# Optimization experiments

Measured on AMD Instinct MI355X. Metric: run time of the kernel, lower is better.

The kernel has to match this reference:

```python
import jax, jax.numpy as jnp
import numpy as np

N = 50000   # nodes
D = 128     # input_dim
E = 1600000 # edges
K = 100     # out_nodes


def setup_inputs() -> dict:
    key = jax.random.key(0)
    ks = jax.random.split(key, 9)
    x = jax.random.normal(ks[0], (N, D), dtype=jnp.float32)
    edge_index = jax.random.randint(ks[1], (2, E), 0, N, dtype=jnp.int64)
    # PyG GCNConv params: Linear(in,out,bias=False) weight + separate bias
    s = 1.0 / np.sqrt(D)
    W1 = jax.random.uniform(ks[2], (D, D), jnp.float32, -s, s)
    b1 = jnp.zeros((D,), jnp.float32)
    W2 = jax.random.uniform(ks[3], (D, D), jnp.float32, -s, s)
    b2 = jnp.zeros((D,), jnp.float32)
    Wa = jax.random.uniform(ks[4], (D, K), jnp.float32, -s, s)
    ba = jax.random.uniform(ks[5], (K,), jnp.float32, -s, s)
    return {"x": x, "edge_index": edge_index, "W1": W1, "b1": b1,
            "W2": W2, "b2": b2, "Wa": Wa, "ba": ba}


def _gcn_conv(x, src, dst, norm, W, b, n_nodes):
    # PyG GCNConv: h = x @ W; aggregate D^-1/2 (A+I) D^-1/2 h; add bias
    h = x @ W                                  # [N, D]
    msg = h[src] * norm[:, None]               # [E+N, D] gather + scale
    agg = jax.ops.segment_sum(msg, dst, num_segments=n_nodes)  # scatter-add
    return agg + b


def reference(x, edge_index, W1, b1, W2, b2, Wa, ba):
    n = x.shape[0]
    loop = jnp.arange(n, dtype=edge_index.dtype)
    src = jnp.concatenate([edge_index[0], loop])   # add self-loops
    dst = jnp.concatenate([edge_index[1], loop])
    deg = jnp.zeros((n,), x.dtype).at[dst].add(1.0)
    dinv = jnp.where(deg > 0, jax.lax.rsqrt(deg), 0.0)
    norm = dinv[src] * dinv[dst]                   # [E+N]

    h = _gcn_conv(x, src, dst, norm, W1, b1, n)
    h = jax.nn.relu(h)
    h = _gcn_conv(h, src, dst, norm, W2, b2, n)
    s = jax.nn.softmax(h @ Wa + ba, axis=1)        # [N, K]
    return s
```

## Files before the change

kernel.cpp:

```cpp
#include <hip/hip_runtime.h>

#define D 128
#define KOUT 100
#define CHUNK 4096

typedef __attribute__((ext_vector_type(8))) short short8;
typedef __attribute__((ext_vector_type(4))) float floatx4;

__device__ inline float bf_lo(unsigned int u) { return __uint_as_float(u << 16); }
__device__ inline float bf_hi(unsigned int u) { return __uint_as_float(u & 0xFFFF0000u); }

__device__ inline unsigned int bf_round(float a) {
    unsigned int ua = __float_as_uint(a);
    return (ua + 0x7FFFu + ((ua >> 16) & 1u)) >> 16;
}
__device__ inline unsigned int pack_bf(float a, float b) {
    return bf_round(a) | (bf_round(b) << 16);
}


__launch_bounds__(256)
__global__ void bucket_pass1(const int* __restrict__ ei, int E, int nbuck, int cap,
                             int* __restrict__ bcur, unsigned int* __restrict__ bdata) {
    __shared__ int hist[256];
    __shared__ int sc[256];
    __shared__ int pfx[256];
    __shared__ int cur[256];
    __shared__ int gbase[256];
    __shared__ unsigned int lbuf[CHUNK];
    __shared__ unsigned char bkt[CHUNK];

    int tid = threadIdx.x;
    int base = blockIdx.x * CHUNK;
    int cnt = E - base; if (cnt > CHUNK) cnt = CHUNK;

    hist[tid] = 0;
    __syncthreads();

    int src[CHUNK / 256];
    int dst[CHUNK / 256];
#pragma unroll
    for (int q = 0; q < CHUNK / 256; q++) {
        int li = tid + q * 256;
        if (li < cnt) {
            src[q] = ei[base + li];
            dst[q] = ei[E + base + li];
            atomicAdd(&hist[dst[q] >> 8], 1);
        }
    }
    __syncthreads();

    int v = hist[tid];
    sc[tid] = v;
    __syncthreads();
    for (int off = 1; off < 256; off <<= 1) {
        int t = (tid >= off) ? sc[tid - off] : 0;
        __syncthreads();
        sc[tid] += t;
        __syncthreads();
    }
    int excl = sc[tid] - v;
    pfx[tid] = excl;
    cur[tid] = excl;
    gbase[tid] = 0;
    if (tid < nbuck && v > 0) gbase[tid] = atomicAdd(&bcur[tid], v);
    __syncthreads();

#pragma unroll
    for (int q = 0; q < CHUNK / 256; q++) {
        int li = tid + q * 256;
        if (li < cnt) {
            int b = dst[q] >> 8;
            int p = atomicAdd(&cur[b], 1);
            lbuf[p] = (unsigned int)src[q] | ((unsigned int)(dst[q] & 255) << 24);
            bkt[p] = (unsigned char)b;
        }
    }
    __syncthreads();

    for (int p = tid; p < cnt; p += 256) {
        int b = bkt[p];
        bdata[(size_t)b * cap + gbase[b] + (p - pfx[b])] = lbuf[p];
    }
}


__launch_bounds__(256)
__global__ void bucket_build(const unsigned int* __restrict__ bdata, const int* __restrict__ bcur,
                             int cap, float* __restrict__ dinv,
                             int* __restrict__ rowptr, int* __restrict__ csr, int n, int nbuck) {
    __shared__ int cnts[256];
    __shared__ int sc[256];
    __shared__ int cur[256];
    __shared__ int bbase;

    int b = blockIdx.x, tid = threadIdx.x;
    if (tid == 0) bbase = 0;
    cnts[tid] = 0;
    __syncthreads();

    int part = 0;
    for (int t = tid; t < b; t += 256) part += bcur[t];
#pragma unroll
    for (int off = 32; off > 0; off >>= 1) part += __shfl_down(part, off);
    if ((tid & 63) == 0 && part != 0) atomicAdd(&bbase, part);

    int cnt = bcur[b];
    const unsigned int* p = bdata + (size_t)b * cap;
    for (int e = tid; e < cnt; e += 256) atomicAdd(&cnts[p[e] >> 24], 1);
    __syncthreads();

    int v = cnts[tid];
    sc[tid] = v;
    __syncthreads();
    for (int off = 1; off < 256; off <<= 1) {
        int t = (tid >= off) ? sc[tid - off] : 0;
        __syncthreads();
        sc[tid] += t;
        __syncthreads();
    }
    int gstart = bbase + (sc[tid] - v);
    int node = b * 256 + tid;
    if (node < n) {
        dinv[node] = rsqrtf((float)(v + 1));
        rowptr[node] = gstart;
    }
    cur[tid] = gstart;
    __syncthreads();

    for (int e = tid; e < cnt; e += 256) {
        unsigned int u = p[e];
        int pos = atomicAdd(&cur[u >> 24], 1);
        csr[pos] = (int)(u & 0xFFFFFFu);
    }
}


__global__ void prep_frag_kernel(const float* __restrict__ W1, const float* __restrict__ W2,
                                 const float* __restrict__ Wa, const float* __restrict__ ba,
                                 unsigned short* __restrict__ Wf1, unsigned short* __restrict__ Wf2,
                                 unsigned short* __restrict__ WfA, float* __restrict__ bpad,
                                 int* __restrict__ bcur, int* __restrict__ rowptr,
                                 unsigned int* __restrict__ zrowA, unsigned int* __restrict__ zrowB,
                                 int n, int E) {
    int idx = blockIdx.x * blockDim.x + threadIdx.x;
    if (idx < 3 * 16384) {
        int m = idx / 16384;
        int e = idx & 16383;
        int j = e & 7, lane = (e >> 3) & 63, ct = (e >> 9) & 7, kt = e >> 12;
        int k = kt * 32 + (lane >> 4) * 8 + j;
        int col = ct * 16 + (lane & 15);
        float val;
        unsigned short* dst;
        if (m == 0)      { val = W1[k * 128 + col]; dst = Wf1; }
        else if (m == 1) { val = W2[k * 128 + col]; dst = Wf2; }
        else             { val = (col < KOUT) ? Wa[k * KOUT + col] : 0.f; dst = WfA; }
        dst[e] = (unsigned short)bf_round(val);
    }
    if (idx < 128) bpad[idx] = (idx < KOUT) ? ba[idx] : 0.f;
    if (idx < 256) bcur[idx] = 0;
    if (idx < 64) { zrowA[idx] = 0u; zrowB[idx] = 0u; }
    if (idx == 256) rowptr[n] = E;
}


__launch_bounds__(256)
__global__ void gemm_mfma_kernel(const void* __restrict__ Xin, const unsigned short* __restrict__ Wf,
                                 const float* __restrict__ bias, const float* __restrict__ oscale,
                                 void* __restrict__ Y, int nrows, int in_bf16, int out_mode) {
    __shared__ float lds_f[64 * 130];
    unsigned short* lds_h = (unsigned short*)lds_f;
    unsigned int* lds_u = (unsigned int*)lds_f;

    int tid = threadIdx.x;
    int w = tid >> 6, lane = tid & 63;
    int quad = lane >> 4, m16 = lane & 15;
    int r0 = blockIdx.x * 64;

    if (!in_bf16) {
        int row = tid >> 2, cg_ = tid & 3;
        bool valid = (r0 + row) < nrows;
        const float4* Xr = (const float4*)Xin + (size_t)(r0 + row) * 32 + cg_ * 8;
#pragma unroll
        for (int j = 0; j < 8; j++) {
            float4 v = valid ? Xr[j] : make_float4(0.f, 0.f, 0.f, 0.f);
            int c = cg_ * 32 + j * 4;
            lds_u[row * 68 + (c >> 1)]     = pack_bf(v.x, v.y);
            lds_u[row * 68 + (c >> 1) + 1] = pack_bf(v.z, v.w);
        }
        __syncthreads();
    }

    floatx4 acc[8];
#pragma unroll
    for (int ct = 0; ct < 8; ct++) acc[ct] = (floatx4){0.f, 0.f, 0.f, 0.f};

    int arow = r0 + w * 16 + m16;
    if (arow > nrows - 1) arow = nrows - 1;
    const unsigned int* Xb = (const unsigned int*)Xin;

    const short8* Wf8 = (const short8*)Wf;
#pragma unroll
    for (int kt = 0; kt < 4; kt++) {
        short8 a;
        if (in_bf16) {
            a = *(const short8*)(Xb + (size_t)arow * 64 + kt * 16 + quad * 4);
        } else {
            a = *(const short8*)(lds_h + (w * 16 + m16) * 136 + kt * 32 + quad * 8);
        }
#pragma unroll
        for (int ct = 0; ct < 8; ct++) {
            short8 b = Wf8[(kt * 8 + ct) * 64 + lane];
            acc[ct] = __builtin_amdgcn_mfma_f32_16x16x32_bf16(a, b, acc[ct], 0, 0, 0);
        }
    }

    if (out_mode == 1) {
        __syncthreads();
#pragma unroll
        for (int ct = 0; ct < 8; ct++) {
#pragma unroll
            for (int r = 0; r < 4; r++) {
                int rl = w * 16 + quad * 4 + r;
                lds_f[rl * 130 + ct * 16 + m16] = acc[ct][r];
            }
        }
        __syncthreads();
        unsigned int* Yb = (unsigned int*)Y;
        for (int r = 0; r < 16; r++) {
            int row = r0 + w * 16 + r;
            if (row < nrows) {
                float sc = oscale ? oscale[row] : 1.f;
                float lo = lds_f[(w * 16 + r) * 130 + 2 * lane] * sc;
                float hi = lds_f[(w * 16 + r) * 130 + 2 * lane + 1] * sc;
                Yb[(size_t)row * 64 + lane] = pack_bf(lo, hi);
            }
        }
    } else {
        float bb[8];
#pragma unroll
        for (int ct = 0; ct < 8; ct++) bb[ct] = bias[ct * 16 + m16];
        float* Yf = (float*)Y;
#pragma unroll
        for (int r = 0; r < 4; r++) {
            int row = r0 + w * 16 + quad * 4 + r;
            float vv[8];
            float mx = -1e30f;
#pragma unroll
            for (int ct = 0; ct < 8; ct++) {
                int col = ct * 16 + m16;
                vv[ct] = (col < KOUT) ? acc[ct][r] + bb[ct] : -1e30f;
                mx = fmaxf(mx, vv[ct]);
            }
#pragma unroll
            for (int off = 1; off < 16; off <<= 1) mx = fmaxf(mx, __shfl_xor(mx, off));
            float se = 0.f;
#pragma unroll
            for (int ct = 0; ct < 8; ct++) {
                vv[ct] = (vv[ct] > -1e29f) ? __expf(vv[ct] - mx) : 0.f;
                se += vv[ct];
            }
#pragma unroll
            for (int off = 1; off < 16; off <<= 1) se += __shfl_xor(se, off);
            float inv = 1.f / se;
            if (row < nrows) {
#pragma unroll
                for (int ct = 0; ct < 8; ct++) {
                    int col = ct * 16 + m16;
                    if (col < KOUT) Yf[(size_t)row * KOUT + col] = vv[ct] * inv;
                }
            }
        }
    }
}


__launch_bounds__(256)
__global__ void aggregate_kernel(const uint4* __restrict__ Hb4, const int* __restrict__ csr,
                                 const int* __restrict__ rowptr,
                                 const float* __restrict__ dinv, const float* __restrict__ bias,
                                 unsigned int* __restrict__ Ob, int n, int do_relu) {
    int wid = threadIdx.x >> 6, lane = threadIdx.x & 63;
    int g = lane >> 4, c = lane & 15;
    int i = blockIdx.x * 4 + wid;
    if (i >= n) return;

    float di = dinv[i];
    int start = rowptr[i];
    int cnt = rowptr[i + 1] - start;
    const int* cp = csr + start;

    float acc[8];
    {
        uint4 sv = Hb4[(size_t)i * 16 + c];
        unsigned int su[4] = {sv.x, sv.y, sv.z, sv.w};
        if (g != 0) { su[0] = su[1] = su[2] = su[3] = 0u; }
#pragma unroll
        for (int t = 0; t < 4; t++) {
            acc[2 * t]     = bf_lo(su[t]);
            acc[2 * t + 1] = bf_hi(su[t]);
        }
    }

    int s[4];
#pragma unroll
    for (int u = 0; u < 4; u++) {
        int idx = u * 4 + g;
        s[u] = (idx < cnt) ? cp[idx] : n;
    }
    for (int e = 0; e < cnt; e += 16) {
        uint4 v[4];
#pragma unroll
        for (int u = 0; u < 4; u++) v[u] = Hb4[(size_t)s[u] * 16 + c];
        int ns[4];
#pragma unroll
        for (int u = 0; u < 4; u++) {
            int idx = e + 16 + u * 4 + g;
            ns[u] = (idx < cnt) ? cp[idx] : n;
        }
#pragma unroll
        for (int u = 0; u < 4; u++) {
            unsigned int uu[4] = {v[u].x, v[u].y, v[u].z, v[u].w};
#pragma unroll
            for (int t = 0; t < 4; t++) {
                acc[2 * t]     += bf_lo(uu[t]);
                acc[2 * t + 1] += bf_hi(uu[t]);
            }
        }
#pragma unroll
        for (int u = 0; u < 4; u++) s[u] = ns[u];
    }

#pragma unroll
    for (int j = 0; j < 8; j++) {
        acc[j] += __shfl_xor(acc[j], 16);
        acc[j] += __shfl_xor(acc[j], 32);
    }

    float2 bb = ((const float2*)bias)[c * 4 + g];
    float fx = acc[g * 2]     * di + bb.x;
    float fy = acc[g * 2 + 1] * di + bb.y;
    if (do_relu) { fx = fmaxf(fx, 0.f); fy = fmaxf(fy, 0.f); }
    Ob[(size_t)i * 64 + c * 4 + g] = pack_bf(fx, fy);
}


extern "C" void kernel_launch(void* const* d_in, const int* in_sizes, int n_in,
                              void* d_out, int out_size, void* d_ws, size_t ws_size,
                              hipStream_t stream) {
    const float* x  = (const float*)d_in[0];
    const int*   ei = (const int*)d_in[1];
    const float* W1 = (const float*)d_in[2];
    const float* b1 = (const float*)d_in[3];
    const float* W2 = (const float*)d_in[4];
    const float* b2 = (const float*)d_in[5];
    const float* Wa = (const float*)d_in[6];
    const float* ba = (const float*)d_in[7];
    float* out = (float*)d_out;

    int N = in_sizes[0] / D;
    int E = in_sizes[1] / 2;

    int nbuck = (N + 255) >> 8;
    int cap = ((E / nbuck) + 2048 + 63) & ~63;

    char* w = (char*)d_ws;
    size_t off = 0;
    auto carve = [&](size_t bytes) -> void* {
        void* p = w + off;
        off = (off + bytes + 255) & ~(size_t)255;
        return p;
    };
    float* dinv   = (float*)carve((size_t)N * 4);
    int*   rowptr = (int*)carve((size_t)(N + 1) * 4);
    int*   bcur   = (int*)carve(256 * 4);
    unsigned int* bdata = (unsigned int*)carve((size_t)nbuck * cap * 4);
    int*   csr    = (int*)carve((size_t)E * 4);
    unsigned short* Wf1 = (unsigned short*)carve(16384 * 2);
    unsigned short* Wf2 = (unsigned short*)carve(16384 * 2);
    unsigned short* WfA = (unsigned short*)carve(16384 * 2);
    float* bpad   = (float*)carve(512);
    unsigned int* HbA = (unsigned int*)carve((size_t)(N + 1) * 64 * 4);
    unsigned int* HbB = (unsigned int*)carve((size_t)(N + 1) * 64 * 4);
    (void)ws_size; (void)n_in; (void)out_size;

    int nbNode4 = (N + 3) / 4;
    int nbGemm = (N + 63) / 64;
    int nbP1 = (E + CHUNK - 1) / CHUNK;

    prep_frag_kernel<<<192, 256, 0, stream>>>(W1, W2, Wa, ba, Wf1, Wf2, WfA, bpad,
                                              bcur, rowptr,
                                              HbA + (size_t)N * 64, HbB + (size_t)N * 64, N, E);
    bucket_pass1<<<nbP1, 256, 0, stream>>>(ei, E, nbuck, cap, bcur, bdata);
    bucket_build<<<nbuck, 256, 0, stream>>>(bdata, bcur, cap, dinv, rowptr, csr, N, nbuck);

    gemm_mfma_kernel<<<nbGemm, 256, 0, stream>>>(x, Wf1, nullptr, dinv, HbA, N, 0, 1);
    aggregate_kernel<<<nbNode4, 256, 0, stream>>>((const uint4*)HbA, csr, rowptr, dinv, b1, HbB, N, 1);
    gemm_mfma_kernel<<<nbGemm, 256, 0, stream>>>(HbB, Wf2, nullptr, dinv, HbA, N, 1, 1);
    aggregate_kernel<<<nbNode4, 256, 0, stream>>>((const uint4*)HbA, csr, rowptr, dinv, b2, HbB, N, 0);
    gemm_mfma_kernel<<<nbGemm, 256, 0, stream>>>(HbB, WfA, bpad, nullptr, out, N, 1, 2);
}
```

Before: 266.7 us.

## Split bf16 feature tables into four column chunks for cache-local aggregation

Stores the intermediate bf16 node features as four column-chunk tables, each (N+1)x32 bf16, instead of row-major 128-wide rows. The GEMM reads and writes are rewritten for this layout. Aggregation now launches four times as many blocks, each handling one chunk with 4-byte gathers, so each pass's gather working set is a quarter of the table and fits better in cache. It also uses nontemporal loads for CSR indices and nontemporal stores for outputs. The cost is that CSR indices are re-read four times and each gather moves less data per request.

```diff
diff --git a/kernel.cpp b/kernel.cpp
--- a/kernel.cpp
+++ b/kernel.cpp
@@ -141,7 +141,7 @@
                                  unsigned short* __restrict__ Wf1, unsigned short* __restrict__ Wf2,
                                  unsigned short* __restrict__ WfA, float* __restrict__ bpad,
                                  int* __restrict__ bcur, int* __restrict__ rowptr,
-                                 unsigned int* __restrict__ zrowA, unsigned int* __restrict__ zrowB,
+                                 unsigned int* __restrict__ HbA, unsigned int* __restrict__ HbB,
                                  int n, int E) {
     int idx = blockIdx.x * blockDim.x + threadIdx.x;
     if (idx < 3 * 16384) {
@@ -159,7 +159,12 @@
     }
     if (idx < 128) bpad[idx] = (idx < KOUT) ? ba[idx] : 0.f;
     if (idx < 256) bcur[idx] = 0;
-    if (idx < 64) { zrowA[idx] = 0u; zrowB[idx] = 0u; }
+    if (idx < 64) {
+        int ch = idx >> 4, cc = idx & 15;
+        size_t zoff = ((size_t)ch * (n + 1) + n) * 16 + cc;
+        HbA[zoff] = 0u;
+        HbB[zoff] = 0u;
+    }
     if (idx == 256) rowptr[n] = E;
 }
 
@@ -176,6 +181,7 @@
     int w = tid >> 6, lane = tid & 63;
     int quad = lane >> 4, m16 = lane & 15;
     int r0 = blockIdx.x * 64;
+    unsigned tstride = (unsigned)(nrows + 1) * 16u;
 
     if (!in_bf16) {
         int row = tid >> 2, cg_ = tid & 3;
@@ -204,7 +210,7 @@
     for (int kt = 0; kt < 4; kt++) {
         short8 a;
         if (in_bf16) {
-            a = *(const short8*)(Xb + (size_t)arow * 64 + kt * 16 + quad * 4);
+            a = *(const short8*)(Xb + (unsigned)kt * tstride + (unsigned)arow * 16u + (unsigned)(quad * 4));
         } else {
             a = *(const short8*)(lds_h + (w * 16 + m16) * 136 + kt * 32 + quad * 8);
         }
@@ -233,7 +239,8 @@
                 float sc = oscale ? oscale[row] : 1.f;
                 float lo = lds_f[(w * 16 + r) * 130 + 2 * lane] * sc;
                 float hi = lds_f[(w * 16 + r) * 130 + 2 * lane + 1] * sc;
-                Yb[(size_t)row * 64 + lane] = pack_bf(lo, hi);
+                Yb[(size_t)(lane >> 4) * tstride + (unsigned)row * 16u + (unsigned)(lane & 15)] =
+                    pack_bf(lo, hi);
             }
         }
     } else {
@@ -276,72 +283,86 @@
 
 
 __launch_bounds__(256)
-__global__ void aggregate_kernel(const uint4* __restrict__ Hb4, const int* __restrict__ csr,
+__global__ void aggregate_kernel(const unsigned int* __restrict__ Hb, const int* __restrict__ csr,
                                  const int* __restrict__ rowptr,
                                  const float* __restrict__ dinv, const float* __restrict__ bias,
                                  unsigned int* __restrict__ Ob, int n, int do_relu) {
     int wid = threadIdx.x >> 6, lane = threadIdx.x & 63;
+    int chunk = blockIdx.x & 3;
+    int i0 = (blockIdx.x >> 2) * 4 + wid;
+    if (i0 >= n) return;
+    int i = __builtin_amdgcn_readfirstlane(i0);
     int g = lane >> 4, c = lane & 15;
-    int i = blockIdx.x * 4 + wid;
-    if (i >= n) return;
+
+    unsigned tstride = (unsigned)(n + 1) * 16u;
+    const unsigned int* T = Hb + (size_t)chunk * tstride;
 
     float di = dinv[i];
     int start = rowptr[i];
     int cnt = rowptr[i + 1] - start;
     const int* cp = csr + start;
 
-    float acc[8];
+    float aLo, aHi;
     {
-        uint4 sv = Hb4[(size_t)i * 16 + c];
-        unsigned int su[4] = {sv.x, sv.y, sv.z, sv.w};
-        if (g != 0) { su[0] = su[1] = su[2] = su[3] = 0u; }
-#pragma unroll
-        for (int t = 0; t < 4; t++) {
-            acc[2 * t]     = bf_lo(su[t]);
-            acc[2 * t + 1] = bf_hi(su[t]);
-        }
-    }
-
-    int s[4];
-#pragma unroll
-    for (int u = 0; u < 4; u++) {
-        int idx = u * 4 + g;
-        s[u] = (idx < cnt) ? cp[idx] : n;
-    }
-    for (int e = 0; e < cnt; e += 16) {
-        uint4 v[4];
-#pragma unroll
-        for (int u = 0; u < 4; u++) v[u] = Hb4[(size_t)s[u] * 16 + c];
-        int ns[4];
-#pragma unroll
-        for (int u = 0; u < 4; u++) {
-            int idx = e + 16 + u * 4 + g;
-            ns[u] = (idx < cnt) ? cp[idx] : n;
-        }
-#pragma unroll
-        for (int u = 0; u < 4; u++) {
-            unsigned int uu[4] = {v[u].x, v[u].y, v[u].z, v[u].w};
-#pragma unroll
-            for (int t = 0; t < 4; t++) {
-                acc[2 * t]     += bf_lo(uu[t]);
-                acc[2 * t + 1] += bf_hi(uu[t]);
-            }
-        }
-#pragma unroll
-        for (int u = 0; u < 4; u++) s[u] = ns[u];
-    }
-
-#pragma unroll
-    for (int j = 0; j < 8; j++) {
-        acc[j] += __shfl_xor(acc[j], 16);
-        acc[j] += __shfl_xor(acc[j], 32);
-    }
-
-    float2 bb = ((const float2*)bias)[c * 4 + g];
-    float fx = acc[g * 2]     * di + bb.x;
-    float fy = acc[g * 2 + 1] * di + bb.y;
-    if (do_relu) { fx = fmaxf(fx, 0.f); fy = fmaxf(fy, 0.f); }
-    Ob[(size_t)i * 64 + c * 4 + g] = pack_bf(fx, fy);
+        unsigned int su = (g == 0) ? T[(unsigned)i * 16u + c] : 0u;
+        aLo = bf_lo(su);
+        aHi = bf_hi(su);
+    }
+
+    int gb = g * 4;
+    int s0 = (gb + 0 < cnt) ? __builtin_nontemporal_load(cp + gb + 0) : n;
+    int s1 = (gb + 1 < cnt) ? __builtin_nontemporal_load(cp + gb + 1) : n;
+    int s2 = (gb + 2 < cnt) ? __builtin_nontemporal_load(cp + gb + 2) : n;
+    int s3 = (gb + 3 < cnt) ? __builtin_nontemporal_load(cp + gb + 3) : n;
+
+    int e = 0;
+    for (; e + 32 <= cnt; e += 16) {
+        unsigned int v0 = T[(unsigned)s0 * 16u + c];
+        unsigned int v1 = T[(unsigned)s1 * 16u + c];
+        unsigned int v2 = T[(unsigned)s2 * 16u + c];
+        unsigned int v3 = T[(unsigned)s3 * 16u + c];
+        int t0 = __builtin_nontemporal_load(cp + e + 16 + gb + 0);
+        int t1 = __builtin_nontemporal_load(cp + e + 16 + gb + 1);
+        int t2 = __builtin_nontemporal_load(cp + e + 16 + gb + 2);
+        int t3 = __builtin_nontemporal_load(cp + e + 16 + gb + 3);
+        float l01 = bf_lo(v0) + bf_lo(v1);
+        float l23 = bf_lo(v2) + bf_lo(v3);
+        float h01 = bf_hi(v0) + bf_hi(v1);
+        float h23 = bf_hi(v2) + bf_hi(v3);
+        aLo += l01 + l23;
+        aHi += h01 + h23;
+        s0 = t0; s1 = t1; s2 = t2; s3 = t3;
+    }
+    for (; e < cnt; e += 16) {
+        unsigned int v0 = T[(unsigned)s0 * 16u + c];
+        unsigned int v1 = T[(unsigned)s1 * 16u + c];
+        unsigned int v2 = T[(unsigned)s2 * 16u + c];
+        unsigned int v3 = T[(unsigned)s3 * 16u + c];
+        int b0 = e + 16 + gb;
+        int t0 = (b0 + 0 < cnt) ? __builtin_nontemporal_load(cp + b0 + 0) : n;
+        int t1 = (b0 + 1 < cnt) ? __builtin_nontemporal_load(cp + b0 + 1) : n;
+        int t2 = (b0 + 2 < cnt) ? __builtin_nontemporal_load(cp + b0 + 2) : n;
+        int t3 = (b0 + 3 < cnt) ? __builtin_nontemporal_load(cp + b0 + 3) : n;
+        float l01 = bf_lo(v0) + bf_lo(v1);
+        float l23 = bf_lo(v2) + bf_lo(v3);
+        float h01 = bf_hi(v0) + bf_hi(v1);
+        float h23 = bf_hi(v2) + bf_hi(v3);
+        aLo += l01 + l23;
+        aHi += h01 + h23;
+        s0 = t0; s1 = t1; s2 = t2; s3 = t3;
+    }
+
+    aLo += __shfl_xor(aLo, 16); aLo += __shfl_xor(aLo, 32);
+    aHi += __shfl_xor(aHi, 16); aHi += __shfl_xor(aHi, 32);
+
+    if (g == 0) {
+        float2 bb = ((const float2*)bias)[chunk * 16 + c];
+        float fx = aLo * di + bb.x;
+        float fy = aHi * di + bb.y;
+        if (do_relu) { fx = fmaxf(fx, 0.f); fy = fmaxf(fy, 0.f); }
+        __builtin_nontemporal_store(pack_bf(fx, fy),
+                                    &Ob[(size_t)chunk * tstride + (unsigned)i * 16u + c]);
+    }
 }
 
 
@@ -389,14 +410,13 @@
     int nbP1 = (E + CHUNK - 1) / CHUNK;
 
     prep_frag_kernel<<<192, 256, 0, stream>>>(W1, W2, Wa, ba, Wf1, Wf2, WfA, bpad,
-                                              bcur, rowptr,
-                                              HbA + (size_t)N * 64, HbB + (size_t)N * 64, N, E);
+                                              bcur, rowptr, HbA, HbB, N, E);
     bucket_pass1<<<nbP1, 256, 0, stream>>>(ei, E, nbuck, cap, bcur, bdata);
     bucket_build<<<nbuck, 256, 0, stream>>>(bdata, bcur, cap, dinv, rowptr, csr, N, nbuck);
 
     gemm_mfma_kernel<<<nbGemm, 256, 0, stream>>>(x, Wf1, nullptr, dinv, HbA, N, 0, 1);
-    aggregate_kernel<<<nbNode4, 256, 0, stream>>>((const uint4*)HbA, csr, rowptr, dinv, b1, HbB, N, 1);
+    aggregate_kernel<<<nbNode4 * 4, 256, 0, stream>>>(HbA, csr, rowptr, dinv, b1, HbB, N, 1);
     gemm_mfma_kernel<<<nbGemm, 256, 0, stream>>>(HbB, Wf2, nullptr, dinv, HbA, N, 1, 1);
-    aggregate_kernel<<<nbNode4, 256, 0, stream>>>((const uint4*)HbA, csr, rowptr, dinv, b2, HbB, N, 0);
+    aggregate_kernel<<<nbNode4 * 4, 256, 0, stream>>>(HbA, csr, rowptr, dinv, b2, HbB, N, 0);
     gemm_mfma_kernel<<<nbGemm, 256, 0, stream>>>(HbB, WfA, bpad, nullptr, out, N, 1, 2);
 }
```

After: 342.2 us. +28.3%, slower.

## Split bf16 feature table into four column chunks for L2-friendly gather

Applied to the files above, without the earlier changes.

Hidden features are now stored as four separate 32-column tables of (N+1) rows instead of one row-major 128-column table. The GEMM writes and reads this chunked layout, and aggregation launches four times as many blocks, each gathering only one 64-byte chunk per neighbor. Each wave handles 16 edges per load with 4 lanes per row, and index loads and output stores become nontemporal. The aim is a smaller working set per pass so the gathered table fits better in cache. The cost is that CSR indices and row pointers are re-read four times and each gather is narrower.

```diff
diff --git a/kernel.cpp b/kernel.cpp
--- a/kernel.cpp
+++ b/kernel.cpp
@@ -6,6 +6,7 @@
 
 typedef __attribute__((ext_vector_type(8))) short short8;
 typedef __attribute__((ext_vector_type(4))) float floatx4;
+typedef __attribute__((ext_vector_type(4))) unsigned int uintx4;
 
 __device__ inline float bf_lo(unsigned int u) { return __uint_as_float(u << 16); }
 __device__ inline float bf_hi(unsigned int u) { return __uint_as_float(u & 0xFFFF0000u); }
@@ -141,7 +142,7 @@
                                  unsigned short* __restrict__ Wf1, unsigned short* __restrict__ Wf2,
                                  unsigned short* __restrict__ WfA, float* __restrict__ bpad,
                                  int* __restrict__ bcur, int* __restrict__ rowptr,
-                                 unsigned int* __restrict__ zrowA, unsigned int* __restrict__ zrowB,
+                                 unsigned int* __restrict__ HbA, unsigned int* __restrict__ HbB,
                                  int n, int E) {
     int idx = blockIdx.x * blockDim.x + threadIdx.x;
     if (idx < 3 * 16384) {
@@ -159,7 +160,12 @@
     }
     if (idx < 128) bpad[idx] = (idx < KOUT) ? ba[idx] : 0.f;
     if (idx < 256) bcur[idx] = 0;
-    if (idx < 64) { zrowA[idx] = 0u; zrowB[idx] = 0u; }
+    if (idx < 64) {
+        int ch = idx >> 4, cc = idx & 15;
+        size_t zoff = ((size_t)ch * (n + 1) + n) * 16 + cc;
+        HbA[zoff] = 0u;
+        HbB[zoff] = 0u;
+    }
     if (idx == 256) rowptr[n] = E;
 }
 
@@ -176,6 +182,7 @@
     int w = tid >> 6, lane = tid & 63;
     int quad = lane >> 4, m16 = lane & 15;
     int r0 = blockIdx.x * 64;
+    unsigned tstride = (unsigned)(nrows + 1) * 16u;
 
     if (!in_bf16) {
         int row = tid >> 2, cg_ = tid & 3;
@@ -204,7 +211,7 @@
     for (int kt = 0; kt < 4; kt++) {
         short8 a;
         if (in_bf16) {
-            a = *(const short8*)(Xb + (size_t)arow * 64 + kt * 16 + quad * 4);
+            a = *(const short8*)(Xb + (unsigned)kt * tstride + (unsigned)arow * 16u + (unsigned)(quad * 4));
         } else {
             a = *(const short8*)(lds_h + (w * 16 + m16) * 136 + kt * 32 + quad * 8);
         }
@@ -233,7 +240,8 @@
                 float sc = oscale ? oscale[row] : 1.f;
                 float lo = lds_f[(w * 16 + r) * 130 + 2 * lane] * sc;
                 float hi = lds_f[(w * 16 + r) * 130 + 2 * lane + 1] * sc;
-                Yb[(size_t)row * 64 + lane] = pack_bf(lo, hi);
+                Yb[(size_t)(lane >> 4) * tstride + (unsigned)row * 16u + (unsigned)(lane & 15)] =
+                    pack_bf(lo, hi);
             }
         }
     } else {
@@ -276,14 +284,19 @@
 
 
 __launch_bounds__(256)
-__global__ void aggregate_kernel(const uint4* __restrict__ Hb4, const int* __restrict__ csr,
+__global__ void aggregate_kernel(const unsigned int* __restrict__ Hb, const int* __restrict__ csr,
                                  const int* __restrict__ rowptr,
                                  const float* __restrict__ dinv, const float* __restrict__ bias,
                                  unsigned int* __restrict__ Ob, int n, int do_relu) {
     int wid = threadIdx.x >> 6, lane = threadIdx.x & 63;
-    int g = lane >> 4, c = lane & 15;
-    int i = blockIdx.x * 4 + wid;
-    if (i >= n) return;
+    int chunk = blockIdx.x & 3;
+    int i0 = (blockIdx.x >> 2) * 4 + wid;
+    if (i0 >= n) return;
+    int i = __builtin_amdgcn_readfirstlane(i0);
+    int e4 = lane >> 2, c4 = lane & 3;
+
+    unsigned tstride = (unsigned)(n + 1) * 16u;
+    const uintx4* T4 = (const uintx4*)(Hb + (size_t)chunk * tstride);
 
     float di = dinv[i];
     int start = rowptr[i];
@@ -292,56 +305,66 @@
 
     float acc[8];
     {
-        uint4 sv = Hb4[(size_t)i * 16 + c];
-        unsigned int su[4] = {sv.x, sv.y, sv.z, sv.w};
-        if (g != 0) { su[0] = su[1] = su[2] = su[3] = 0u; }
+        uintx4 sv = (e4 == 0) ? T4[(unsigned)i * 4u + (unsigned)c4]
+                              : (uintx4){0u, 0u, 0u, 0u};
 #pragma unroll
         for (int t = 0; t < 4; t++) {
-            acc[2 * t]     = bf_lo(su[t]);
-            acc[2 * t + 1] = bf_hi(su[t]);
-        }
-    }
-
-    int s[4];
-#pragma unroll
-    for (int u = 0; u < 4; u++) {
-        int idx = u * 4 + g;
-        s[u] = (idx < cnt) ? cp[idx] : n;
-    }
-    for (int e = 0; e < cnt; e += 16) {
-        uint4 v[4];
-#pragma unroll
-        for (int u = 0; u < 4; u++) v[u] = Hb4[(size_t)s[u] * 16 + c];
-        int ns[4];
-#pragma unroll
-        for (int u = 0; u < 4; u++) {
-            int idx = e + 16 + u * 4 + g;
-            ns[u] = (idx < cnt) ? cp[idx] : n;
-        }
-#pragma unroll
-        for (int u = 0; u < 4; u++) {
-            unsigned int uu[4] = {v[u].x, v[u].y, v[u].z, v[u].w};
-#pragma unroll
-            for (int t = 0; t < 4; t++) {
-                acc[2 * t]     += bf_lo(uu[t]);
-                acc[2 * t + 1] += bf_hi(uu[t]);
-            }
-        }
-#pragma unroll
-        for (int u = 0; u < 4; u++) s[u] = ns[u];
+            acc[2 * t]     = bf_lo(sv[t]);
+            acc[2 * t + 1] = bf_hi(sv[t]);
+        }
+    }
+
+    int s0 = (e4 < cnt)      ? __builtin_nontemporal_load(cp + e4)      : n;
+    int s1 = (16 + e4 < cnt) ? __builtin_nontemporal_load(cp + 16 + e4) : n;
+
+    int e = 0;
+    for (; e + 64 <= cnt; e += 32) {
+        uintx4 v0 = T4[(unsigned)s0 * 4u + (unsigned)c4];
+        uintx4 v1 = T4[(unsigned)s1 * 4u + (unsigned)c4];
+        int t0 = __builtin_nontemporal_load(cp + e + 32 + e4);
+        int t1 = __builtin_nontemporal_load(cp + e + 48 + e4);
+#pragma unroll
+        for (int t = 0; t < 4; t++) {
+            acc[2 * t]     += bf_lo(v0[t]) + bf_lo(v1[t]);
+            acc[2 * t + 1] += bf_hi(v0[t]) + bf_hi(v1[t]);
+        }
+        s0 = t0; s1 = t1;
+    }
+    for (; e < cnt; e += 32) {
+        uintx4 v0 = T4[(unsigned)s0 * 4u + (unsigned)c4];
+        uintx4 v1 = T4[(unsigned)s1 * 4u + (unsigned)c4];
+        int b0 = e + 32 + e4, b1 = e + 48 + e4;
+        int t0 = (b0 < cnt) ? __builtin_nontemporal_load(cp + b0) : n;
+        int t1 = (b1 < cnt) ? __builtin_nontemporal_load(cp + b1) : n;
+#pragma unroll
+        for (int t = 0; t < 4; t++) {
+            acc[2 * t]     += bf_lo(v0[t]) + bf_lo(v1[t]);
+            acc[2 * t + 1] += bf_hi(v0[t]) + bf_hi(v1[t]);
+        }
+        s0 = t0; s1 = t1;
     }
 
 #pragma unroll
     for (int j = 0; j < 8; j++) {
+        acc[j] += __shfl_xor(acc[j], 4);
+        acc[j] += __shfl_xor(acc[j], 8);
         acc[j] += __shfl_xor(acc[j], 16);
         acc[j] += __shfl_xor(acc[j], 32);
     }
 
-    float2 bb = ((const float2*)bias)[c * 4 + g];
-    float fx = acc[g * 2]     * di + bb.x;
-    float fy = acc[g * 2 + 1] * di + bb.y;
-    if (do_relu) { fx = fmaxf(fx, 0.f); fy = fmaxf(fy, 0.f); }
-    Ob[(size_t)i * 64 + c * 4 + g] = pack_bf(fx, fy);
+    if (e4 == 0) {
+        uintx4 ov;
+#pragma unroll
+        for (int t = 0; t < 4; t++) {
+            float2 bb = ((const float2*)bias)[chunk * 16 + c4 * 4 + t];
+            float fx = acc[2 * t]     * di + bb.x;
+            float fy = acc[2 * t + 1] * di + bb.y;
+            if (do_relu) { fx = fmaxf(fx, 0.f); fy = fmaxf(fy, 0.f); }
+            ov[t] = pack_bf(fx, fy);
+        }
+        __builtin_nontemporal_store(ov,
+            (uintx4*)(Ob + (size_t)chunk * tstride + (unsigned)i * 16u + (unsigned)(c4 * 4)));
+    }
 }
 
 
@@ -389,14 +412,13 @@
     int nbP1 = (E + CHUNK - 1) / CHUNK;
 
     prep_frag_kernel<<<192, 256, 0, stream>>>(W1, W2, Wa, ba, Wf1, Wf2, WfA, bpad,
-                                              bcur, rowptr,
-                                              HbA + (size_t)N * 64, HbB + (size_t)N * 64, N, E);
+                                              bcur, rowptr, HbA, HbB, N, E);
     bucket_pass1<<<nbP1, 256, 0, stream>>>(ei, E, nbuck, cap, bcur, bdata);
     bucket_build<<<nbuck, 256, 0, stream>>>(bdata, bcur, cap, dinv, rowptr, csr, N, nbuck);
 
     gemm_mfma_kernel<<<nbGemm, 256, 0, stream>>>(x, Wf1, nullptr, dinv, HbA, N, 0, 1);
-    aggregate_kernel<<<nbNode4, 256, 0, stream>>>((const uint4*)HbA, csr, rowptr, dinv, b1, HbB, N, 1);
+    aggregate_kernel<<<nbNode4 * 4, 256, 0, stream>>>(HbA, csr, rowptr, dinv, b1, HbB, N, 1);
     gemm_mfma_kernel<<<nbGemm, 256, 0, stream>>>(HbB, Wf2, nullptr, dinv, HbA, N, 1, 1);
-    aggregate_kernel<<<nbNode4, 256, 0, stream>>>((const uint4*)HbA, csr, rowptr, dinv, b2, HbB, N, 0);
+    aggregate_kernel<<<nbNode4 * 4, 256, 0, stream>>>(HbA, csr, rowptr, dinv, b2, HbB, N, 0);
     gemm_mfma_kernel<<<nbGemm, 256, 0, stream>>>(HbB, WfA, bpad, nullptr, out, N, 1, 2);
 }
```

After: 345.1 us. 29.4% more time.
